# Performance work log

Hardware: AMD Instinct MI355X
Metric: run time of the kernel (lower is better)

Reference implementation:

```python
import jax, jax.numpy as jnp
import numpy as np

N = 8192
IN_DIM = 128
OUT_DIM = 128
EDGE_P = 0.002  # avg degree ~16


def setup_inputs() -> dict:
    key = jax.random.key(0)
    k1, k2, k3, k4 = jax.random.split(key, 4)
    H = jax.random.normal(k1, (N, IN_DIM), dtype=jnp.float32)
    # dense binary adjacency (module expects a dense N x N float tensor)
    A = (jax.random.uniform(k2, (N, N)) < EDGE_P).astype(jnp.float32)
    # nn.Linear params: weight [out, in] (xavier_uniform), bias [out]
    limit = np.sqrt(6.0 / (IN_DIM + OUT_DIM)).astype(np.float32)
    W = jax.random.uniform(k3, (OUT_DIM, IN_DIM), minval=-limit, maxval=limit, dtype=jnp.float32)
    bound = 1.0 / np.sqrt(IN_DIM)
    b = jax.random.uniform(k4, (OUT_DIM,), minval=-bound, maxval=bound, dtype=jnp.float32)
    return {"H": H, "A": A, "W": W, "b": b}


def reference(H, A, W, b):
    n = A.shape[0]
    A_t = A + jnp.eye(n, dtype=A.dtype)          # A + I
    D = A_t.sum(axis=1)                          # degree
    D_inv = jnp.where(D > 0, D ** -0.5, jnp.zeros_like(D))
    # diag(D_inv) @ A_t @ diag(D_inv) == broadcasted row/col scaling
    A_norm = D_inv[:, None] * A_t * D_inv[None, :]
    HW = H @ W.T + b                             # Linear(H): [N, out_dim]
    return jax.nn.relu(A_norm @ HW)
```

## Files before the change

kernel.cpp:

```cpp
#include <hip/hip_runtime.h>
#include <hip/hip_bf16.h>
#include <math.h>

#define N 8192
#define DIM 128
#define CAP 256
#define LROWS 8

typedef float v4f __attribute__((ext_vector_type(4)));

__global__ __launch_bounds__(256) void scan_kernel(
    const float* __restrict__ A, const float* __restrict__ W,
    unsigned short* __restrict__ idx, int* __restrict__ cnt,
    float* __restrict__ dinv, float* __restrict__ Wt) {
  int row = blockIdx.x;
  int tid = threadIdx.x;
  __shared__ int lcnt;
  if (tid == 0) lcnt = 0;
  __syncthreads();

  if (row < DIM && tid < DIM) {
    Wt[row * DIM + tid] = W[tid * DIM + row];
  }

  const v4f* Arow = (const v4f*)(A + (size_t)row * N);
  unsigned short* myidx = idx + (size_t)row * CAP;
#pragma unroll
  for (int it = 0; it < 8; ++it) {
    v4f v = __builtin_nontemporal_load(&Arow[it * 256 + tid]);
    int cbase = (it * 256 + tid) * 4;
    if (v.x != 0.0f) { int s = atomicAdd(&lcnt, 1); if (s < CAP) myidx[s] = (unsigned short)(cbase    ); }
    if (v.y != 0.0f) { int s = atomicAdd(&lcnt, 1); if (s < CAP) myidx[s] = (unsigned short)(cbase + 1); }
    if (v.z != 0.0f) { int s = atomicAdd(&lcnt, 1); if (s < CAP) myidx[s] = (unsigned short)(cbase + 2); }
    if (v.w != 0.0f) { int s = atomicAdd(&lcnt, 1); if (s < CAP) myidx[s] = (unsigned short)(cbase + 3); }
  }
  __syncthreads();
  if (tid == 0) {
    int c = lcnt; if (c > CAP) c = CAP;
    cnt[row] = c;
    dinv[row] = rsqrtf((float)(lcnt + 1));
  }
}

__global__ __launch_bounds__(128) void linear_kernel(
    const float* __restrict__ H, const float* __restrict__ Wt,
    const float* __restrict__ b, const float* __restrict__ dinv,
    float* __restrict__ G) {
  __shared__ float Hl[LROWS][DIM];
  int k = threadIdx.x;
  int r0 = blockIdx.x * LROWS;

  const float4* Hg = (const float4*)(H + (size_t)r0 * DIM);
  float4* Hl4 = (float4*)&Hl[0][0];
#pragma unroll
  for (int it = 0; it < LROWS / 4; ++it) Hl4[it * 128 + k] = Hg[it * 128 + k];
  __syncthreads();

  float acc[LROWS];
#pragma unroll
  for (int r = 0; r < LROWS; ++r) acc[r] = 0.0f;

#pragma unroll 4
  for (int m = 0; m < DIM; ++m) {
    float w = Wt[m * DIM + k];
#pragma unroll
    for (int r = 0; r < LROWS; ++r) acc[r] += Hl[r][m] * w;
  }

  float bk = b[k];
#pragma unroll
  for (int r = 0; r < LROWS; ++r) {
    G[(size_t)(r0 + r) * DIM + k] = dinv[r0 + r] * (acc[r] + bk);
  }
}

__global__ __launch_bounds__(128) void gather_kernel(
    const float* __restrict__ G, const unsigned short* __restrict__ idx,
    const int* __restrict__ cnt, const float* __restrict__ dinv,
    float* __restrict__ out) {
  int row = blockIdx.x;
  int k = threadIdx.x;
  __shared__ unsigned short lidx[CAP];
  int c = cnt[row];
  const unsigned short* myidx = idx + (size_t)row * CAP;
  for (int t = k; t < c; t += 128) lidx[t] = myidx[t];
  __syncthreads();

  float acc = G[(size_t)row * DIM + k];
  int t = 0;
  for (; t + 4 <= c; t += 4) {
    int j0 = lidx[t], j1 = lidx[t + 1], j2 = lidx[t + 2], j3 = lidx[t + 3];
    float g0 = G[(size_t)j0 * DIM + k];
    float g1 = G[(size_t)j1 * DIM + k];
    float g2 = G[(size_t)j2 * DIM + k];
    float g3 = G[(size_t)j3 * DIM + k];
    acc += ((g0 + g1) + (g2 + g3));
  }
  for (; t < c; ++t) acc += G[(size_t)lidx[t] * DIM + k];

  float v = dinv[row] * acc;
  out[(size_t)row * DIM + k] = v > 0.0f ? v : 0.0f;
}

extern "C" void kernel_launch(void* const* d_in, const int* in_sizes, int n_in,
                              void* d_out, int out_size, void* d_ws, size_t ws_size,
                              hipStream_t stream) {
  const float* H = (const float*)d_in[0];
  const float* A = (const float*)d_in[1];
  const float* W = (const float*)d_in[2];
  const float* b = (const float*)d_in[3];
  float* out = (float*)d_out;

  char* ws = (char*)d_ws;
  size_t off = 0;
  float* G = (float*)(ws + off);              off += (size_t)N * DIM * sizeof(float);
  float* dinv = (float*)(ws + off);           off += (size_t)N * sizeof(float);
  int* cnt = (int*)(ws + off);                off += (size_t)N * sizeof(int);
  unsigned short* idx = (unsigned short*)(ws + off); off += (size_t)N * CAP * sizeof(unsigned short);
  float* Wt = (float*)(ws + off);             off += (size_t)DIM * DIM * sizeof(float);

  scan_kernel<<<N, 256, 0, stream>>>(A, W, idx, cnt, dinv, Wt);
  linear_kernel<<<N / LROWS, 128, 0, stream>>>(H, Wt, b, dinv, G);
  gather_kernel<<<N, 128, 0, stream>>>(G, idx, cnt, dinv, out);
}
```

Before: 356.2 us.

## Fuse adjacency scan and linear into one launch, move dinv scaling to gather

The adjacency scan and the linear layer are merged into one grid. The first blocks compute H·W^T+b directly from W rows, with no transposed copy, and the remaining blocks scan A rows. Because the linear no longer depends on dinv, the degree scaling of neighbour features moves into the gather kernel, which reads dinv per neighbour. This removes a launch and the Wt transpose, and lets the compute-bound linear overlap with the bandwidth-bound scan, at the cost of extra dinv loads in the gather.

```diff
diff --git a/kernel.cpp b/kernel.cpp
--- a/kernel.cpp
+++ b/kernel.cpp
@@ -5,72 +5,72 @@
 #define N 8192
 #define DIM 128
 #define CAP 256
-#define LROWS 8
+#define LIN_ROWS 16
+#define LIN_BLOCKS (N / LIN_ROWS)
 
 typedef float v4f __attribute__((ext_vector_type(4)));
 
-__global__ __launch_bounds__(256) void scan_kernel(
-    const float* __restrict__ A, const float* __restrict__ W,
+__global__ __launch_bounds__(256) void fused_kernel(
+    const float* __restrict__ A, const float* __restrict__ H,
+    const float* __restrict__ W, const float* __restrict__ b,
     unsigned short* __restrict__ idx, int* __restrict__ cnt,
-    float* __restrict__ dinv, float* __restrict__ Wt) {
-  int row = blockIdx.x;
+    float* __restrict__ dinv, float* __restrict__ G) {
+  __shared__ float Hl[LIN_ROWS][DIM];
+  int bid = blockIdx.x;
   int tid = threadIdx.x;
-  __shared__ int lcnt;
-  if (tid == 0) lcnt = 0;
-  __syncthreads();
 
-  if (row < DIM && tid < DIM) {
-    Wt[row * DIM + tid] = W[tid * DIM + row];
-  }
+  if (bid < LIN_BLOCKS) {
+    int r0 = bid * LIN_ROWS;
+    const float4* Hg = (const float4*)(H + (size_t)r0 * DIM);
+    float4* Hl4 = (float4*)&Hl[0][0];
+    Hl4[tid] = Hg[tid];
+    Hl4[tid + 256] = Hg[tid + 256];
+    __syncthreads();
 
-  const v4f* Arow = (const v4f*)(A + (size_t)row * N);
-  unsigned short* myidx = idx + (size_t)row * CAP;
+    int half = tid >> 7;
+    int k = tid & 127;
+    int rbase = half * 8;
+    const float4* Wk = (const float4*)(W + (size_t)k * DIM);
+    float bk = b[k];
+    float acc[8];
 #pragma unroll
-  for (int it = 0; it < 8; ++it) {
-    v4f v = __builtin_nontemporal_load(&Arow[it * 256 + tid]);
-    int cbase = (it * 256 + tid) * 4;
-    if (v.x != 0.0f) { int s = atomicAdd(&lcnt, 1); if (s < CAP) myidx[s] = (unsigned short)(cbase    ); }
-    if (v.y != 0.0f) { int s = atomicAdd(&lcnt, 1); if (s < CAP) myidx[s] = (unsigned short)(cbase + 1); }
-    if (v.z != 0.0f) { int s = atomicAdd(&lcnt, 1); if (s < CAP) myidx[s] = (unsigned short)(cbase + 2); }
-    if (v.w != 0.0f) { int s = atomicAdd(&lcnt, 1); if (s < CAP) myidx[s] = (unsigned short)(cbase + 3); }
-  }
-  __syncthreads();
-  if (tid == 0) {
-    int c = lcnt; if (c > CAP) c = CAP;
-    cnt[row] = c;
-    dinv[row] = rsqrtf((float)(lcnt + 1));
-  }
-}
-
-__global__ __launch_bounds__(128) void linear_kernel(
-    const float* __restrict__ H, const float* __restrict__ Wt,
-    const float* __restrict__ b, const float* __restrict__ dinv,
-    float* __restrict__ G) {
-  __shared__ float Hl[LROWS][DIM];
-  int k = threadIdx.x;
-  int r0 = blockIdx.x * LROWS;
-
-  const float4* Hg = (const float4*)(H + (size_t)r0 * DIM);
-  float4* Hl4 = (float4*)&Hl[0][0];
-#pragma unroll
-  for (int it = 0; it < LROWS / 4; ++it) Hl4[it * 128 + k] = Hg[it * 128 + k];
-  __syncthreads();
-
-  float acc[LROWS];
-#pragma unroll
-  for (int r = 0; r < LROWS; ++r) acc[r] = 0.0f;
+    for (int r = 0; r < 8; ++r) acc[r] = 0.0f;
 
 #pragma unroll 4
-  for (int m = 0; m < DIM; ++m) {
-    float w = Wt[m * DIM + k];
+    for (int m4 = 0; m4 < DIM / 4; ++m4) {
+      float4 w4 = Wk[m4];
 #pragma unroll
-    for (int r = 0; r < LROWS; ++r) acc[r] += Hl[r][m] * w;
-  }
+      for (int r = 0; r < 8; ++r) {
+        float4 h4 = ((const float4*)&Hl[rbase + r][0])[m4];
+        acc[r] += h4.x * w4.x + h4.y * w4.y + h4.z * w4.z + h4.w * w4.w;
+      }
+    }
+#pragma unroll
+    for (int r = 0; r < 8; ++r)
+      G[(size_t)(r0 + rbase + r) * DIM + k] = acc[r] + bk;
+  } else {
+    int row = bid - LIN_BLOCKS;
+    int* lcnt = (int*)&Hl[0][0];
+    if (tid == 0) *lcnt = 0;
+    __syncthreads();
 
-  float bk = b[k];
+    const v4f* Arow = (const v4f*)(A + (size_t)row * N);
+    unsigned short* myidx = idx + (size_t)row * CAP;
 #pragma unroll
-  for (int r = 0; r < LROWS; ++r) {
-    G[(size_t)(r0 + r) * DIM + k] = dinv[r0 + r] * (acc[r] + bk);
+    for (int it = 0; it < 8; ++it) {
+      v4f v = __builtin_nontemporal_load(&Arow[it * 256 + tid]);
+      int cbase = (it * 256 + tid) * 4;
+      if (v.x != 0.0f) { int s = atomicAdd(lcnt, 1); if (s < CAP) myidx[s] = (unsigned short)(cbase    ); }
+      if (v.y != 0.0f) { int s = atomicAdd(lcnt, 1); if (s < CAP) myidx[s] = (unsigned short)(cbase + 1); }
+      if (v.z != 0.0f) { int s = atomicAdd(lcnt, 1); if (s < CAP) myidx[s] = (unsigned short)(cbase + 2); }
+      if (v.w != 0.0f) { int s = atomicAdd(lcnt, 1); if (s < CAP) myidx[s] = (unsigned short)(cbase + 3); }
+    }
+    __syncthreads();
+    if (tid == 0) {
+      int c = *lcnt; if (c > CAP) c = CAP;
+      cnt[row] = c;
+      dinv[row] = rsqrtf((float)(*lcnt + 1));
+    }
   }
 }
 
@@ -86,19 +86,20 @@
   for (int t = k; t < c; t += 128) lidx[t] = myidx[t];
   __syncthreads();
 
-  float acc = G[(size_t)row * DIM + k];
+  float di = dinv[row];
+  float acc = di * G[(size_t)row * DIM + k];
   int t = 0;
   for (; t + 4 <= c; t += 4) {
     int j0 = lidx[t], j1 = lidx[t + 1], j2 = lidx[t + 2], j3 = lidx[t + 3];
-    float g0 = G[(size_t)j0 * DIM + k];
-    float g1 = G[(size_t)j1 * DIM + k];
-    float g2 = G[(size_t)j2 * DIM + k];
-    float g3 = G[(size_t)j3 * DIM + k];
+    float g0 = dinv[j0] * G[(size_t)j0 * DIM + k];
+    float g1 = dinv[j1] * G[(size_t)j1 * DIM + k];
+    float g2 = dinv[j2] * G[(size_t)j2 * DIM + k];
+    float g3 = dinv[j3] * G[(size_t)j3 * DIM + k];
     acc += ((g0 + g1) + (g2 + g3));
   }
-  for (; t < c; ++t) acc += G[(size_t)lidx[t] * DIM + k];
+  for (; t < c; ++t) acc += dinv[lidx[t]] * G[(size_t)lidx[t] * DIM + k];
 
-  float v = dinv[row] * acc;
+  float v = di * acc;
   out[(size_t)row * DIM + k] = v > 0.0f ? v : 0.0f;
 }
 
@@ -117,9 +118,7 @@
   float* dinv = (float*)(ws + off);           off += (size_t)N * sizeof(float);
   int* cnt = (int*)(ws + off);                off += (size_t)N * sizeof(int);
   unsigned short* idx = (unsigned short*)(ws + off); off += (size_t)N * CAP * sizeof(unsigned short);
-  float* Wt = (float*)(ws + off);             off += (size_t)DIM * DIM * sizeof(float);
 
-  scan_kernel<<<N, 256, 0, stream>>>(A, W, idx, cnt, dinv, Wt);
-  linear_kernel<<<N / LROWS, 128, 0, stream>>>(H, Wt, b, dinv, G);
+  fused_kernel<<<LIN_BLOCKS + N, 256, 0, stream>>>(A, H, W, b, idx, cnt, dinv, G);
   gather_kernel<<<N, 128, 0, stream>>>(G, idx, cnt, dinv, out);
 }
```

New measurement: 354.6 us. Within noise of the previous version (-0.4%).
